# Kernel optimization log

Measured on AMD Instinct MI355X. Metric: run time of the kernel, lower is better.

Reference implementation:

```python
import jax, jax.numpy as jnp
import numpy as np

B, N, H, L = 4, 200, 128, 3
HH = H // 2
VOC_E_IN, VOC_E_OUT, NODE_DIM = 3, 2, 2
EPS_BN = 1e-5


def masked_bn(x, m, gamma, beta):
    """BatchNorm1d (batch stats, no running stats) applied only to masked positions.
    x: (..., H), m: (...) float mask. Unmasked entries pass through unchanged."""
    mm = m[..., None]
    cnt = jnp.sum(m)
    axes = tuple(range(x.ndim - 1))
    mean = jnp.sum(x * mm, axis=axes) / cnt
    var = jnp.sum(((x - mean) ** 2) * mm, axis=axes) / cnt  # biased, as BatchNorm1d
    xn = (x - mean) * jax.lax.rsqrt(var + EPS_BN) * gamma + beta
    return jnp.where(mm > 0, xn, x)


def gcn_layer(x, e, mask, sq_mask, p, i):
    # EdgeFeatures: e_ij = U*e_ij + V*x_i + V*x_j (V*x masked)
    Ue = jnp.einsum('bijh,hk->bijk', e, p['eU_w'][i]) + p['eU_b'][i]
    Vx_e = mask[..., None] * (jnp.einsum('bnh,hk->bnk', x, p['eV_w'][i]) + p['eV_b'][i])
    e_tmp = Ue + Vx_e[:, :, None, :] + Vx_e[:, None, :, :]
    gate = jax.nn.sigmoid(e_tmp)
    # NodeFeatures (mean aggregation)
    Ux = mask[..., None] * (jnp.einsum('bnh,hk->bnk', x, p['nU_w'][i]) + p['nU_b'][i])
    Vx = mask[..., None] * (jnp.einsum('bnh,hk->bnk', x, p['nV_w'][i]) + p['nV_b'][i])
    gate_m = gate * sq_mask[..., None]
    agg = jnp.einsum('bijh,bjh->bih', gate_m, Vx)
    denom = jnp.sum(gate_m, axis=2)
    x_tmp = Ux + agg / (1e-20 + denom)
    # masked batchnorm + ReLU + residual
    e_bn = masked_bn(e_tmp, sq_mask, p['bnE_g'][i], p['bnE_b'][i])
    x_bn = masked_bn(x_tmp, mask, p['bnN_g'][i], p['bnN_b'][i])
    return x + jax.nn.relu(x_bn), e + jax.nn.relu(e_bn)


def forward(x_edges, x_edges_values, x_nodes_coord, mask, p):
    x = jnp.einsum('bnd,dh->bnh', x_nodes_coord, p['w_coord'])          # (B,N,H)
    e_val = x_edges_values[..., None] * p['w_eval'][0]                  # (B,N,N,HH)
    e_tag = p['emb_edge'][x_edges]                                      # (B,N,N,HH)
    e = jnp.concatenate([e_val, e_tag], axis=-1)                        # (B,N,N,H)
    sq_mask = mask[:, :, None] * mask[:, None, :]
    for i in range(L):
        x, e = gcn_layer(x, e, mask, sq_mask, p, i)
    # MLP on edges (mlp_layers=2 -> one hidden ReLU layer)
    h = jax.nn.relu(jnp.einsum('bijh,hk->bijk', e, p['mlp_U_w']) + p['mlp_U_b'])
    y = jnp.einsum('bijh,hk->bijk', h, p['mlp_V_w']) + p['mlp_V_b']     # (B,N,N,2)
    return y


def setup_inputs() -> dict:
    key = jax.random.key(0)
    ks = jax.random.split(key, 32)
    x_edges = jax.random.randint(ks[0], (B, N, N), 0, VOC_E_IN)
    x_edges_values = jax.random.uniform(ks[1], (B, N, N), dtype=jnp.float32)
    x_nodes_coord = jax.random.uniform(ks[2], (B, N, NODE_DIM), dtype=jnp.float32)
    # prefix mask: variable graph sizes padded to N (as ConvTSP builds)
    lens = jax.random.randint(ks[3], (B,), N // 2, N + 1)
    mask = (jnp.arange(N)[None, :] < lens[:, None]).astype(jnp.float32)
    s = 1.0 / np.sqrt(H)
    inp = dict(x_edges=x_edges, x_edges_values=x_edges_values,
               x_nodes_coord=x_nodes_coord, mask=mask,
               w_coord=jax.random.normal(ks[4], (NODE_DIM, H)) * 0.5,
               w_eval=jax.random.normal(ks[5], (1, HH)) * 0.5,
               emb_edge=jax.random.normal(ks[6], (VOC_E_IN, HH)) * 0.5,
               eU_w=jax.random.normal(ks[7], (L, H, H)) * s,
               eU_b=jnp.zeros((L, H)),
               eV_w=jax.random.normal(ks[8], (L, H, H)) * s,
               eV_b=jnp.zeros((L, H)),
               nU_w=jax.random.normal(ks[9], (L, H, H)) * s,
               nU_b=jnp.zeros((L, H)),
               nV_w=jax.random.normal(ks[10], (L, H, H)) * s,
               nV_b=jnp.zeros((L, H)),
               bnE_g=jnp.ones((L, H)), bnE_b=jnp.zeros((L, H)),
               bnN_g=jnp.ones((L, H)), bnN_b=jnp.zeros((L, H)),
               mlp_U_w=jax.random.normal(ks[11], (H, H)) * s,
               mlp_U_b=jnp.zeros((H,)),
               mlp_V_w=jax.random.normal(ks[12], (H, VOC_E_OUT)) * s,
               mlp_V_b=jnp.zeros((VOC_E_OUT,)))
    return inp


def reference(x_edges, x_edges_values, x_nodes_coord, mask,
              w_coord, w_eval, emb_edge,
              eU_w, eU_b, eV_w, eV_b, nU_w, nU_b, nV_w, nV_b,
              bnE_g, bnE_b, bnN_g, bnN_b,
              mlp_U_w, mlp_U_b, mlp_V_w, mlp_V_b):
    p = dict(w_coord=w_coord, w_eval=w_eval, emb_edge=emb_edge,
             eU_w=eU_w, eU_b=eU_b, eV_w=eV_w, eV_b=eV_b,
             nU_w=nU_w, nU_b=nU_b, nV_w=nV_w, nV_b=nV_b,
             bnE_g=bnE_g, bnE_b=bnE_b, bnN_g=bnN_g, bnN_b=bnN_b,
             mlp_U_w=mlp_U_w, mlp_U_b=mlp_U_b, mlp_V_w=mlp_V_w, mlp_V_b=mlp_V_b)
    return forward(x_edges, x_edges_values, x_nodes_coord, mask, p)
```

## Files before the change

kernel.cpp:

```cpp
#include <hip/hip_runtime.h>
#include <hip/hip_bf16.h>


typedef __hip_bfloat16 bf16;
typedef __attribute__((ext_vector_type(8))) short short8_t;
typedef __attribute__((ext_vector_type(4))) float f32x4;

#define B_ 4
#define N_ 200
#define H_ 128
#define BN_ (B_ * N_)
#define MT_ 13
#define MROWS_ 208

__device__ __forceinline__ unsigned short f2b(float f) {
  unsigned int i = __float_as_uint(f);
  i = (i + 0x7fffu + ((i >> 16) & 1u)) >> 16;
  return (unsigned short)i;
}
__device__ __forceinline__ float b2f16(unsigned short u) {
  return __uint_as_float((unsigned int)u << 16);
}


__global__ __launch_bounds__(128) void k_init_x(
    const float* __restrict__ coord, const float* __restrict__ w_coord,
    float* __restrict__ x) {
  int bi = blockIdx.x, h = threadIdx.x;
  float c0 = coord[bi * 2 + 0], c1 = coord[bi * 2 + 1];
  x[(size_t)bi * H_ + h] = c0 * w_coord[h] + c1 * w_coord[H_ + h];
}

__global__ __launch_bounds__(256) void k_cnt(const float* __restrict__ mask,
                                             float* __restrict__ cnts) {
  int t = threadIdx.x, b = t >> 6, l = t & 63;
  float s = 0.f;
  for (int n = l; n < N_; n += 64) s += mask[b * N_ + n];
#pragma unroll
  for (int d = 1; d < 64; d <<= 1) s += __shfl_xor(s, d);
  __shared__ float ms[B_];
  if (l == 0) ms[b] = s;
  __syncthreads();
  if (t == 0) {
    float cn = 0.f, ce = 0.f;
    for (int k = 0; k < B_; ++k) { cn += ms[k]; ce += ms[k] * ms[k]; }
    cnts[0] = cn; cnts[1] = ce;
  }
}

__global__ __launch_bounds__(256) void k_prep_w(const float* __restrict__ eUw,
                                                const float* __restrict__ mUw,
                                                bf16* __restrict__ WT) {
  int blk = blockIdx.x;
  const float* src = (blk < 3) ? (eUw + (size_t)blk * H_ * H_) : mUw;
  bf16* dst = WT + (size_t)blk * H_ * H_;
  for (int q = threadIdx.x; q < H_ * H_; q += 256) {
    int out = q >> 7, in = q & 127;
    dst[q] = __float2bfloat16(src[in * H_ + out]);
  }
}


__global__ __launch_bounds__(128) void k_node_lin(
    const float* __restrict__ x, const float* __restrict__ eVw,
    const float* __restrict__ eVb, const float* __restrict__ nUw,
    const float* __restrict__ nUb, const float* __restrict__ nVw,
    const float* __restrict__ nVb, const float* __restrict__ mask,
    float* __restrict__ Vxe, float* __restrict__ Ux, float* __restrict__ Vx) {
  __shared__ float xr[H_];
  int bi = blockIdx.x, h = threadIdx.x;
  xr[h] = x[(size_t)bi * H_ + h];
  __syncthreads();
  float m = mask[bi];
  float a = 0.f, bvv = 0.f, c = 0.f;
#pragma unroll 4
  for (int k = 0; k < H_; ++k) {
    float xv = xr[k];
    a   = fmaf(xv, eVw[k * H_ + h], a);
    bvv = fmaf(xv, nUw[k * H_ + h], bvv);
    c   = fmaf(xv, nVw[k * H_ + h], c);
  }
  Vxe[(size_t)bi * H_ + h] = m * (a + eVb[h]);
  Ux[(size_t)bi * H_ + h]  = m * (bvv + nUb[h]);
  Vx[(size_t)bi * H_ + h]  = m * (c + nVb[h]);
}


#define LDS_PUT(SA, ROW, K0, V)                                            \
  {                                                                        \
    unsigned int p0 = ((unsigned int)f2b((V).y) << 16) | f2b((V).x);       \
    unsigned int p1 = ((unsigned int)f2b((V).w) << 16) | f2b((V).z);       \
    unsigned long long pk = ((unsigned long long)p1 << 32) | p0;           \
    int byo = ((ROW) << 8) + ((((K0) * 2)) ^ (((ROW) & 7) << 4));          \
    *(unsigned long long*)((SA) + byo) = pk;                               \
  }


template <int MODE>
__global__ __launch_bounds__(256, 3) void k_edge(
    float* __restrict__ e, bf16* __restrict__ etmp,
    const float* __restrict__ ssPrev, const int* __restrict__ xe,
    const float* __restrict__ ev, const float* __restrict__ w_eval,
    const float* __restrict__ emb, const bf16* __restrict__ WT,
    const float* __restrict__ eUb, const float* __restrict__ Vxe,
    const float* __restrict__ Vx, const float* __restrict__ Ux,
    const float* __restrict__ mask, float* __restrict__ xtmp,
    float* __restrict__ sums) {
  __shared__ __align__(16) char sA[MROWS_ * 256];
  const int bi = blockIdx.x;
  const int b = bi / N_;
  const int t = threadIdx.x;
  const int lane = t & 63;
  const int w = t >> 6;
  const float mask_i = mask[bi];

  const int n0 = w << 5;
  const int colA = n0 + (lane & 15);
  const int colB = colA + 16;
  const int kgrp = (lane >> 4) << 3;
  short8_t bfA[4], bfB[4];
  {
    const short* w0 = (const short*)WT + colA * H_ + kgrp;
    const short* w1 = (const short*)WT + colB * H_ + kgrp;
#pragma unroll
    for (int kk = 0; kk < 4; ++kk) {
      bfA[kk] = *(const short8_t*)(w0 + kk * 32);
      bfB[kk] = *(const short8_t*)(w1 + kk * 32);
    }
  }

  {
    float* eb = e + (size_t)bi * N_ * H_;
    const unsigned short* tb =
        (const unsigned short*)etmp + (size_t)bi * N_ * H_;
    for (int q4 = t; q4 < MROWS_ * 32; q4 += 256) {
      int row = q4 >> 5, k0 = (q4 & 31) << 2;
      float4 v = make_float4(0.f, 0.f, 0.f, 0.f);
      if (row < N_) {
        if (MODE == 0) {
          if (k0 < 64) {
            float evv = ev[bi * N_ + row];
            v.x = evv * w_eval[k0 + 0];
            v.y = evv * w_eval[k0 + 1];
            v.z = evv * w_eval[k0 + 2];
            v.w = evv * w_eval[k0 + 3];
          } else {
            v = *(const float4*)(emb + xe[bi * N_ + row] * 64 + (k0 - 64));
          }
        } else {
          v = *(const float4*)(eb + row * H_ + k0);
          ushort4 tv = *(const ushort4*)(tb + row * H_ + k0);
          float mj = mask[b * N_ + row];
          bool msk = (mask_i * mj) > 0.f;
          float4 sc = *(const float4*)(ssPrev + k0);
          float4 sh = *(const float4*)(ssPrev + H_ + k0);
          float f0 = b2f16(tv.x), f1 = b2f16(tv.y);
          float f2 = b2f16(tv.z), f3 = b2f16(tv.w);
          v.x += fmaxf(msk ? fmaf(f0, sc.x, sh.x) : f0, 0.f);
          v.y += fmaxf(msk ? fmaf(f1, sc.y, sh.y) : f1, 0.f);
          v.z += fmaxf(msk ? fmaf(f2, sc.z, sh.z) : f2, 0.f);
          v.w += fmaxf(msk ? fmaf(f3, sc.w, sh.w) : f3, 0.f);
        }
        *(float4*)(eb + row * H_ + k0) = v;
      }
      LDS_PUT(sA, row, k0, v)
    }
  }
  __syncthreads();

  const float add0 = eUb[colA] + Vxe[(size_t)bi * H_ + colA];
  const float add1 = eUb[colB] + Vxe[(size_t)bi * H_ + colB];
  const float* VxeB = Vxe + (size_t)b * N_ * H_;
  const float* VxB  = Vx  + (size_t)b * N_ * H_;

  float agg0 = 0.f, agg1 = 0.f, den0 = 0.f, den1 = 0.f;
  float s1a = 0.f, s1b = 0.f, s2a = 0.f, s2b = 0.f;
  const int kb = (lane >> 4) << 4;

  for (int mt = 0; mt < MT_; ++mt) {
    f32x4 acc0 = {0.f, 0.f, 0.f, 0.f}, acc1 = {0.f, 0.f, 0.f, 0.f};
    int ra = mt * 16 + (lane & 15);
#pragma unroll
    for (int kk = 0; kk < 4; ++kk) {
      int ko = kk * 64 + kb;
      short8_t av = *(const short8_t*)(sA + (ra << 8) + (ko ^ ((ra & 7) << 4)));
      acc0 = __builtin_amdgcn_mfma_f32_16x16x32_bf16(av, bfA[kk], acc0, 0, 0, 0);
      acc1 = __builtin_amdgcn_mfma_f32_16x16x32_bf16(av, bfB[kk], acc1, 0, 0, 0);
    }
#pragma unroll
    for (int r = 0; r < 4; ++r) {
      int j = mt * 16 + ((lane >> 4) << 2) + r;
      bool valid = (j < N_);
      float mj = valid ? mask[b * N_ + j] : 0.f;
      float sqm = mask_i * mj;
      float vj0 = valid ? VxeB[(size_t)j * H_ + colA] : 0.f;
      float vj1 = valid ? VxeB[(size_t)j * H_ + colB] : 0.f;
      float t0 = acc0[r] + add0 + vj0;
      float t1 = acc1[r] + add1 + vj1;
      if (valid) {
        size_t o = ((size_t)bi * N_ + j) * H_;
        etmp[o + colA] = __float2bfloat16(t0);
        etmp[o + colB] = __float2bfloat16(t1);
      }
      float g0 = sqm / (1.f + __expf(-t0));
      float g1 = sqm / (1.f + __expf(-t1));
      float vx0 = valid ? VxB[(size_t)j * H_ + colA] : 0.f;
      float vx1 = valid ? VxB[(size_t)j * H_ + colB] : 0.f;
      agg0 = fmaf(g0, vx0, agg0);
      agg1 = fmaf(g1, vx1, agg1);
      den0 += g0; den1 += g1;
      s1a = fmaf(t0, sqm, s1a);
      s1b = fmaf(t1, sqm, s1b);
      s2a = fmaf(t0 * sqm, t0, s2a);
      s2b = fmaf(t1 * sqm, t1, s2b);
    }
  }
#pragma unroll
  for (int d = 16; d <= 32; d <<= 1) {
    agg0 += __shfl_xor(agg0, d); agg1 += __shfl_xor(agg1, d);
    den0 += __shfl_xor(den0, d); den1 += __shfl_xor(den1, d);
    s1a += __shfl_xor(s1a, d);   s1b += __shfl_xor(s1b, d);
    s2a += __shfl_xor(s2a, d);   s2b += __shfl_xor(s2b, d);
  }
  if ((lane >> 4) == 0) {
    atomicAdd(&sums[colA], s1a);
    atomicAdd(&sums[colB], s1b);
    atomicAdd(&sums[H_ + colA], s2a);
    atomicAdd(&sums[H_ + colB], s2b);
    float xt0 = Ux[(size_t)bi * H_ + colA] + agg0 / (1e-20f + den0);
    float xt1 = Ux[(size_t)bi * H_ + colB] + agg1 / (1e-20f + den1);
    xtmp[(size_t)bi * H_ + colA] = xt0;
    xtmp[(size_t)bi * H_ + colB] = xt1;
    atomicAdd(&sums[2 * H_ + colA], xt0 * mask_i);
    atomicAdd(&sums[3 * H_ + colA], xt0 * xt0 * mask_i);
    atomicAdd(&sums[2 * H_ + colB], xt1 * mask_i);
    atomicAdd(&sums[3 * H_ + colB], xt1 * xt1 * mask_i);
  }
}


__global__ __launch_bounds__(128) void k_stats(
    const float* __restrict__ sums, const float* __restrict__ cnts,
    const float* __restrict__ gE, const float* __restrict__ bE,
    const float* __restrict__ gN, const float* __restrict__ bN,
    float* __restrict__ ss) {
  int h = threadIdx.x;
  float cntN = cnts[0], cntE = cnts[1];
  float mE = sums[h] / cntE;
  float vE = sums[H_ + h] / cntE - mE * mE;
  float scE = gE[h] * rsqrtf(vE + 1e-5f);
  ss[h] = scE;
  ss[H_ + h] = bE[h] - mE * scE;
  float mN = sums[2 * H_ + h] / cntN;
  float vN = sums[3 * H_ + h] / cntN - mN * mN;
  float scN = gN[h] * rsqrtf(vN + 1e-5f);
  ss[2 * H_ + h] = scN;
  ss[3 * H_ + h] = bN[h] - mN * scN;
}

__global__ __launch_bounds__(128) void k_xupd(const float* __restrict__ xtmp,
                                              const float* __restrict__ mask,
                                              const float* __restrict__ ss,
                                              float* __restrict__ x) {
  int bi = blockIdx.x, h = threadIdx.x;
  float mi = mask[bi];
  float tv = xtmp[(size_t)bi * H_ + h];
  float xn = (mi > 0.f) ? fmaf(tv, ss[2 * H_ + h], ss[3 * H_ + h]) : tv;
  x[(size_t)bi * H_ + h] += fmaxf(xn, 0.f);
}


__global__ __launch_bounds__(256, 2) void k_head(
    const float* __restrict__ e, const bf16* __restrict__ etmp,
    const float* __restrict__ ssPrev, const bf16* __restrict__ UT,
    const float* __restrict__ Ub, const float* __restrict__ Vw,
    const float* __restrict__ Vb, const float* __restrict__ mask,
    float* __restrict__ y) {
  __shared__ __align__(16) char sA[MROWS_ * 256];
  __shared__ float part[4][MROWS_][2];
  const int bi = blockIdx.x;
  const int b = bi / N_;
  const int t = threadIdx.x;
  const int lane = t & 63;
  const int w = t >> 6;
  const float mask_i = mask[bi];

  const int n0 = w << 5;
  const int colA = n0 + (lane & 15);
  const int colB = colA + 16;
  const int kgrp = (lane >> 4) << 3;
  short8_t bfA[4], bfB[4];
  {
    const short* w0 = (const short*)UT + colA * H_ + kgrp;
    const short* w1 = (const short*)UT + colB * H_ + kgrp;
#pragma unroll
    for (int kk = 0; kk < 4; ++kk) {
      bfA[kk] = *(const short8_t*)(w0 + kk * 32);
      bfB[kk] = *(const short8_t*)(w1 + kk * 32);
    }
  }

  {
    const float* eb = e + (size_t)bi * N_ * H_;
    const unsigned short* tb =
        (const unsigned short*)etmp + (size_t)bi * N_ * H_;
    for (int q4 = t; q4 < MROWS_ * 32; q4 += 256) {
      int row = q4 >> 5, k0 = (q4 & 31) << 2;
      float4 v = make_float4(0.f, 0.f, 0.f, 0.f);
      if (row < N_) {
        v = *(const float4*)(eb + row * H_ + k0);
        ushort4 tv = *(const ushort4*)(tb + row * H_ + k0);
        float mj = mask[b * N_ + row];
        bool msk = (mask_i * mj) > 0.f;
        float4 sc = *(const float4*)(ssPrev + k0);
        float4 sh = *(const float4*)(ssPrev + H_ + k0);
        float f0 = b2f16(tv.x), f1 = b2f16(tv.y);
        float f2 = b2f16(tv.z), f3 = b2f16(tv.w);
        v.x += fmaxf(msk ? fmaf(f0, sc.x, sh.x) : f0, 0.f);
        v.y += fmaxf(msk ? fmaf(f1, sc.y, sh.y) : f1, 0.f);
        v.z += fmaxf(msk ? fmaf(f2, sc.z, sh.z) : f2, 0.f);
        v.w += fmaxf(msk ? fmaf(f3, sc.w, sh.w) : f3, 0.f);
      }
      LDS_PUT(sA, row, k0, v)
    }
  }
  __syncthreads();

  float bu0 = Ub[colA], bu1 = Ub[colB];
  float v00 = Vw[colA * 2], v01 = Vw[colA * 2 + 1];
  float v10 = Vw[colB * 2], v11 = Vw[colB * 2 + 1];
  const int kb = (lane >> 4) << 4;

  for (int mt = 0; mt < MT_; ++mt) {
    f32x4 acc0 = {0.f, 0.f, 0.f, 0.f}, acc1 = {0.f, 0.f, 0.f, 0.f};
    int ra = mt * 16 + (lane & 15);
#pragma unroll
    for (int kk = 0; kk < 4; ++kk) {
      int ko = kk * 64 + kb;
      short8_t av = *(const short8_t*)(sA + (ra << 8) + (ko ^ ((ra & 7) << 4)));
      acc0 = __builtin_amdgcn_mfma_f32_16x16x32_bf16(av, bfA[kk], acc0, 0, 0, 0);
      acc1 = __builtin_amdgcn_mfma_f32_16x16x32_bf16(av, bfB[kk], acc1, 0, 0, 0);
    }
#pragma unroll
    for (int r = 0; r < 4; ++r) {
      float h0v = fmaxf(acc0[r] + bu0, 0.f);
      float h1v = fmaxf(acc1[r] + bu1, 0.f);
      float p0 = h0v * v00 + h1v * v10;
      float p1 = h0v * v01 + h1v * v11;
#pragma unroll
      for (int d = 1; d < 16; d <<= 1) {
        p0 += __shfl_xor(p0, d);
        p1 += __shfl_xor(p1, d);
      }
      int j = mt * 16 + ((lane >> 4) << 2) + r;
      if ((lane & 15) == 0) { part[w][j][0] = p0; part[w][j][1] = p1; }
    }
  }
  __syncthreads();
  float vb0 = Vb[0], vb1 = Vb[1];
  for (int q = t; q < N_ * 2; q += 256) {
    int j = q >> 1, c = q & 1;
    float s = part[0][j][c] + part[1][j][c] + part[2][j][c] + part[3][j][c] +
              (c ? vb1 : vb0);
    y[((size_t)bi * N_ + j) * 2 + c] = s;
  }
}


extern "C" void kernel_launch(void* const* d_in, const int* in_sizes, int n_in,
                              void* d_out, int out_size, void* d_ws,
                              size_t ws_size, hipStream_t stream) {
  const int*   x_edges = (const int*)d_in[0];
  const float* ev      = (const float*)d_in[1];
  const float* coord   = (const float*)d_in[2];
  const float* mask    = (const float*)d_in[3];
  const float* w_coord = (const float*)d_in[4];
  const float* w_eval  = (const float*)d_in[5];
  const float* emb     = (const float*)d_in[6];
  const float* eUw = (const float*)d_in[7];
  const float* eUb = (const float*)d_in[8];
  const float* eVw = (const float*)d_in[9];
  const float* eVb = (const float*)d_in[10];
  const float* nUw = (const float*)d_in[11];
  const float* nUb = (const float*)d_in[12];
  const float* nVw = (const float*)d_in[13];
  const float* nVb = (const float*)d_in[14];
  const float* gE  = (const float*)d_in[15];
  const float* bE  = (const float*)d_in[16];
  const float* gN  = (const float*)d_in[17];
  const float* bN  = (const float*)d_in[18];
  const float* mUw = (const float*)d_in[19];
  const float* mUb = (const float*)d_in[20];
  const float* mVw = (const float*)d_in[21];
  const float* mVb = (const float*)d_in[22];

  char* ws = (char*)d_ws;
  size_t off = 0;
  auto alloc = [&](size_t bytes) {
    void* p = ws + off;
    off += (bytes + 255) & ~(size_t)255;
    return p;
  };
  float* e    = (float*)alloc((size_t)B_ * N_ * N_ * H_ * 4);
  bf16* etmp  = (bf16*)alloc((size_t)B_ * N_ * N_ * H_ * 2);
  float* x    = (float*)alloc((size_t)BN_ * H_ * 4);
  float* Vxe  = (float*)alloc((size_t)BN_ * H_ * 4);
  float* Ux   = (float*)alloc((size_t)BN_ * H_ * 4);
  float* Vx   = (float*)alloc((size_t)BN_ * H_ * 4);
  float* xtmp = (float*)alloc((size_t)BN_ * H_ * 4);
  float* sums = (float*)alloc(4 * H_ * 4);
  float* ss   = (float*)alloc(4 * H_ * 4);
  float* cnts = (float*)alloc(256);
  bf16* WT    = (bf16*)alloc((size_t)4 * H_ * H_ * 2);

  k_prep_w<<<4, 256, 0, stream>>>(eUw, mUw, WT);
  k_init_x<<<BN_, 128, 0, stream>>>(coord, w_coord, x);
  k_cnt<<<1, 256, 0, stream>>>(mask, cnts);

  for (int l = 0; l < 3; ++l) {
    size_t wo = (size_t)l * H_ * H_;
    size_t bo = (size_t)l * H_;
    hipMemsetAsync(sums, 0, 4 * H_ * 4, stream);
    k_node_lin<<<BN_, 128, 0, stream>>>(x, eVw + wo, eVb + bo, nUw + wo,
                                        nUb + bo, nVw + wo, nVb + bo, mask,
                                        Vxe, Ux, Vx);
    if (l == 0) {
      k_edge<0><<<BN_, 256, 0, stream>>>(e, etmp, ss, x_edges, ev, w_eval,
                                         emb, WT + wo, eUb + bo, Vxe, Vx, Ux,
                                         mask, xtmp, sums);
    } else {
      k_edge<1><<<BN_, 256, 0, stream>>>(e, etmp, ss, x_edges, ev, w_eval,
                                         emb, WT + wo, eUb + bo, Vxe, Vx, Ux,
                                         mask, xtmp, sums);
    }
    k_stats<<<1, 128, 0, stream>>>(sums, cnts, gE + bo, bE + bo, gN + bo,
                                   bN + bo, ss);
    if (l < 2) k_xupd<<<BN_, 128, 0, stream>>>(xtmp, mask, ss, x);
  }
  k_head<<<BN_, 256, 0, stream>>>(e, etmp, ss, WT + (size_t)3 * H_ * H_, mUb,
                                  mVw, mVb, mask, (float*)d_out);
}
```

Measured before the change: 405.3 us.

## Store edge state in bf16, recompute layer-0 edges, fuse BN stats into consumers

The edge tensor e is now stored in bf16 instead of fp32, which halves its global read and write traffic. Layer 0 no longer writes e at all; layer 1 rebuilds the initial edge embedding on the fly (MODE 2) before adding the normalized residual. The separate k_stats and k_xupd kernels and the per-layer memsets are removed. The BN scale and shift are now recomputed from the raw sums inside k_node_lin, k_edge and k_head, and the last layer skips the unused node-update work. The edge loop also prefetches the next tile's Vxe, Vx and mask values and widens the prologue to 8-element vectors, at the cost of rounding the residual edge state to bf16.

```diff
diff --git a/kernel.cpp b/kernel.cpp
--- a/kernel.cpp
+++ b/kernel.cpp
@@ -61,24 +61,40 @@
 }
 
 
+template <int UPD>
 __global__ __launch_bounds__(128) void k_node_lin(
-    const float* __restrict__ x, const float* __restrict__ eVw,
-    const float* __restrict__ eVb, const float* __restrict__ nUw,
-    const float* __restrict__ nUb, const float* __restrict__ nVw,
-    const float* __restrict__ nVb, const float* __restrict__ mask,
-    float* __restrict__ Vxe, float* __restrict__ Ux, float* __restrict__ Vx) {
+    float* __restrict__ x, const float* __restrict__ xtmp,
+    const float* __restrict__ sumsPrev, const float* __restrict__ cnts,
+    const float* __restrict__ gNp, const float* __restrict__ bNp,
+    const float* __restrict__ eVw, const float* __restrict__ eVb,
+    const float* __restrict__ nUw, const float* __restrict__ nUb,
+    const float* __restrict__ nVw, const float* __restrict__ nVb,
+    const float* __restrict__ mask, float* __restrict__ Vxe,
+    float* __restrict__ Ux, float* __restrict__ Vx) {
   __shared__ float xr[H_];
   int bi = blockIdx.x, h = threadIdx.x;
-  xr[h] = x[(size_t)bi * H_ + h];
+  float m = mask[bi];
+  float xv = x[(size_t)bi * H_ + h];
+  if (UPD) {
+    float cntN = cnts[0];
+    float mN = sumsPrev[256 + h] / cntN;
+    float vN = sumsPrev[384 + h] / cntN - mN * mN;
+    float scN = gNp[h] * rsqrtf(vN + 1e-5f);
+    float shN = bNp[h] - mN * scN;
+    float tv = xtmp[(size_t)bi * H_ + h];
+    float xn = (m > 0.f) ? fmaf(tv, scN, shN) : tv;
+    xv += fmaxf(xn, 0.f);
+    x[(size_t)bi * H_ + h] = xv;
+  }
+  xr[h] = xv;
   __syncthreads();
-  float m = mask[bi];
   float a = 0.f, bvv = 0.f, c = 0.f;
 #pragma unroll 4
   for (int k = 0; k < H_; ++k) {
-    float xv = xr[k];
-    a   = fmaf(xv, eVw[k * H_ + h], a);
-    bvv = fmaf(xv, nUw[k * H_ + h], bvv);
-    c   = fmaf(xv, nVw[k * H_ + h], c);
+    float kx = xr[k];
+    a   = fmaf(kx, eVw[k * H_ + h], a);
+    bvv = fmaf(kx, nUw[k * H_ + h], bvv);
+    c   = fmaf(kx, nVw[k * H_ + h], c);
   }
   Vxe[(size_t)bi * H_ + h] = m * (a + eVb[h]);
   Ux[(size_t)bi * H_ + h]  = m * (bvv + nUb[h]);
@@ -86,27 +102,40 @@
 }
 
 
-#define LDS_PUT(SA, ROW, K0, V)                                            \
-  {                                                                        \
-    unsigned int p0 = ((unsigned int)f2b((V).y) << 16) | f2b((V).x);       \
-    unsigned int p1 = ((unsigned int)f2b((V).w) << 16) | f2b((V).z);       \
-    unsigned long long pk = ((unsigned long long)p1 << 32) | p0;           \
-    int byo = ((ROW) << 8) + ((((K0) * 2)) ^ (((ROW) & 7) << 4));          \
-    *(unsigned long long*)((SA) + byo) = pk;                               \
-  }
-
-
-template <int MODE>
+__device__ __forceinline__ void load_pre(int mt, int jg, int bN, float mask_i,
+                                         const float* __restrict__ mask,
+                                         const float* __restrict__ VxeB,
+                                         const float* __restrict__ VxB,
+                                         int colA, int colB, float* vj0,
+                                         float* vj1, float* vx0, float* vx1,
+                                         float* sq) {
+#pragma unroll
+  for (int r = 0; r < 4; ++r) {
+    int j = (mt << 4) + jg + r;
+    bool valid = (j < N_);
+    float mj = valid ? mask[bN + j] : 0.f;
+    sq[r] = mask_i * mj;
+    vj0[r] = valid ? VxeB[(size_t)j * H_ + colA] : 0.f;
+    vj1[r] = valid ? VxeB[(size_t)j * H_ + colB] : 0.f;
+    vx0[r] = valid ? VxB[(size_t)j * H_ + colA] : 0.f;
+    vx1[r] = valid ? VxB[(size_t)j * H_ + colB] : 0.f;
+  }
+}
+
+
+template <int MODE, bool DO_X>
 __global__ __launch_bounds__(256, 3) void k_edge(
-    float* __restrict__ e, bf16* __restrict__ etmp,
-    const float* __restrict__ ssPrev, const int* __restrict__ xe,
-    const float* __restrict__ ev, const float* __restrict__ w_eval,
-    const float* __restrict__ emb, const bf16* __restrict__ WT,
-    const float* __restrict__ eUb, const float* __restrict__ Vxe,
-    const float* __restrict__ Vx, const float* __restrict__ Ux,
-    const float* __restrict__ mask, float* __restrict__ xtmp,
-    float* __restrict__ sums) {
+    bf16* __restrict__ e, bf16* __restrict__ etmp,
+    const float* __restrict__ sumsPrev, const float* __restrict__ cnts,
+    const float* __restrict__ gEp, const float* __restrict__ bEp,
+    const int* __restrict__ xe, const float* __restrict__ ev,
+    const float* __restrict__ w_eval, const float* __restrict__ emb,
+    const bf16* __restrict__ WT, const float* __restrict__ eUb,
+    const float* __restrict__ Vxe, const float* __restrict__ Vx,
+    const float* __restrict__ Ux, const float* __restrict__ mask,
+    float* __restrict__ xtmp, float* __restrict__ sumsCur) {
   __shared__ __align__(16) char sA[MROWS_ * 256];
+  __shared__ float ssE_s[256];
   const int bi = blockIdx.x;
   const int b = bi / N_;
   const int t = threadIdx.x;
@@ -114,8 +143,17 @@
   const int w = t >> 6;
   const float mask_i = mask[bi];
 
-  const int n0 = w << 5;
-  const int colA = n0 + (lane & 15);
+  if (MODE != 0) {
+    int h = t & 127;
+    float cntE = cnts[1];
+    float mE = sumsPrev[h] / cntE;
+    float vE = sumsPrev[128 + h] / cntE - mE * mE;
+    float scE = gEp[h] * rsqrtf(vE + 1e-5f);
+    ssE_s[t] = (t < 128) ? scE : (bEp[h] - mE * scE);
+    __syncthreads();
+  }
+
+  const int colA = (w << 5) + (lane & 15);
   const int colB = colA + 16;
   const int kgrp = (lane >> 4) << 3;
   short8_t bfA[4], bfB[4];
@@ -130,40 +168,79 @@
   }
 
   {
-    float* eb = e + (size_t)bi * N_ * H_;
+    const int k0 = (t & 15) << 3;
+    const int lr0 = t >> 4;
+    float scr[8], shr[8], we[8];
+    if (MODE != 0) {
+#pragma unroll
+      for (int c = 0; c < 8; ++c) {
+        scr[c] = ssE_s[k0 + c];
+        shr[c] = ssE_s[128 + k0 + c];
+      }
+    }
+    if ((MODE == 0 || MODE == 2) && k0 < 64) {
+#pragma unroll
+      for (int c = 0; c < 8; ++c) we[c] = w_eval[k0 + c];
+    }
+    unsigned short* eb = (unsigned short*)e + (size_t)bi * N_ * H_;
     const unsigned short* tb =
         (const unsigned short*)etmp + (size_t)bi * N_ * H_;
-    for (int q4 = t; q4 < MROWS_ * 32; q4 += 256) {
-      int row = q4 >> 5, k0 = (q4 & 31) << 2;
-      float4 v = make_float4(0.f, 0.f, 0.f, 0.f);
+#pragma unroll
+    for (int n = 0; n < 13; ++n) {
+      int row = lr0 + (n << 4);
+      float v[8];
+#pragma unroll
+      for (int c = 0; c < 8; ++c) v[c] = 0.f;
       if (row < N_) {
-        if (MODE == 0) {
+        if (MODE == 0 || MODE == 2) {
           if (k0 < 64) {
             float evv = ev[bi * N_ + row];
-            v.x = evv * w_eval[k0 + 0];
-            v.y = evv * w_eval[k0 + 1];
-            v.z = evv * w_eval[k0 + 2];
-            v.w = evv * w_eval[k0 + 3];
+#pragma unroll
+            for (int c = 0; c < 8; ++c) v[c] = evv * we[c];
           } else {
-            v = *(const float4*)(emb + xe[bi * N_ + row] * 64 + (k0 - 64));
+            const float* em = emb + xe[bi * N_ + row] * 64 + (k0 - 64);
+            float4 a4 = *(const float4*)em;
+            float4 b4 = *(const float4*)(em + 4);
+            v[0] = a4.x; v[1] = a4.y; v[2] = a4.z; v[3] = a4.w;
+            v[4] = b4.x; v[5] = b4.y; v[6] = b4.z; v[7] = b4.w;
           }
         } else {
-          v = *(const float4*)(eb + row * H_ + k0);
-          ushort4 tv = *(const ushort4*)(tb + row * H_ + k0);
+          uint4 e8 = *(const uint4*)(eb + row * H_ + k0);
+          v[0] = b2f16((unsigned short)e8.x);
+          v[1] = b2f16((unsigned short)(e8.x >> 16));
+          v[2] = b2f16((unsigned short)e8.y);
+          v[3] = b2f16((unsigned short)(e8.y >> 16));
+          v[4] = b2f16((unsigned short)e8.z);
+          v[5] = b2f16((unsigned short)(e8.z >> 16));
+          v[6] = b2f16((unsigned short)e8.w);
+          v[7] = b2f16((unsigned short)(e8.w >> 16));
+        }
+        if (MODE != 0) {
+          uint4 t8 = *(const uint4*)(tb + row * H_ + k0);
           float mj = mask[b * N_ + row];
           bool msk = (mask_i * mj) > 0.f;
-          float4 sc = *(const float4*)(ssPrev + k0);
-          float4 sh = *(const float4*)(ssPrev + H_ + k0);
-          float f0 = b2f16(tv.x), f1 = b2f16(tv.y);
-          float f2 = b2f16(tv.z), f3 = b2f16(tv.w);
-          v.x += fmaxf(msk ? fmaf(f0, sc.x, sh.x) : f0, 0.f);
-          v.y += fmaxf(msk ? fmaf(f1, sc.y, sh.y) : f1, 0.f);
-          v.z += fmaxf(msk ? fmaf(f2, sc.z, sh.z) : f2, 0.f);
-          v.w += fmaxf(msk ? fmaf(f3, sc.w, sh.w) : f3, 0.f);
+          unsigned short tu[8] = {
+              (unsigned short)t8.x, (unsigned short)(t8.x >> 16),
+              (unsigned short)t8.y, (unsigned short)(t8.y >> 16),
+              (unsigned short)t8.z, (unsigned short)(t8.z >> 16),
+              (unsigned short)t8.w, (unsigned short)(t8.w >> 16)};
+#pragma unroll
+          for (int c = 0; c < 8; ++c) {
+            float f = b2f16(tu[c]);
+            float xn = msk ? fmaf(f, scr[c], shr[c]) : f;
+            v[c] += fmaxf(xn, 0.f);
+          }
         }
-        *(float4*)(eb + row * H_ + k0) = v;
       }
-      LDS_PUT(sA, row, k0, v)
+      uint4 pk;
+      pk.x = ((unsigned int)f2b(v[1]) << 16) | f2b(v[0]);
+      pk.y = ((unsigned int)f2b(v[3]) << 16) | f2b(v[2]);
+      pk.z = ((unsigned int)f2b(v[5]) << 16) | f2b(v[4]);
+      pk.w = ((unsigned int)f2b(v[7]) << 16) | f2b(v[6]);
+      if (MODE != 0 && row < N_)
+        *(uint4*)(eb + row * H_ + k0) = pk;
+      int byo = (row << 8) + ((k0 * 2) ^ ((row & 7) << 4));
+      *(uint4*)(sA + byo) = pk;
     }
   }
   __syncthreads();
@@ -172,14 +249,22 @@
   const float add1 = eUb[colB] + Vxe[(size_t)bi * H_ + colB];
   const float* VxeB = Vxe + (size_t)b * N_ * H_;
   const float* VxB  = Vx  + (size_t)b * N_ * H_;
+  const int bN = b * N_;
+  const int jg = (lane >> 4) << 2;
+  const int kb = (lane >> 4) << 4;
 
   float agg0 = 0.f, agg1 = 0.f, den0 = 0.f, den1 = 0.f;
   float s1a = 0.f, s1b = 0.f, s2a = 0.f, s2b = 0.f;
-  const int kb = (lane >> 4) << 4;
-
+
+  float cvj0[4], cvj1[4], cvx0[4], cvx1[4], csq[4];
+  float nvj0[4], nvj1[4], nvx0[4], nvx1[4], nsq[4];
+  load_pre(0, jg, bN, mask_i, mask, VxeB, VxB, colA, colB, cvj0, cvj1, cvx0,
+           cvx1, csq);
+
+#pragma unroll
   for (int mt = 0; mt < MT_; ++mt) {
     f32x4 acc0 = {0.f, 0.f, 0.f, 0.f}, acc1 = {0.f, 0.f, 0.f, 0.f};
-    int ra = mt * 16 + (lane & 15);
+    int ra = (mt << 4) + (lane & 15);
 #pragma unroll
     for (int kk = 0; kk < 4; ++kk) {
       int ko = kk * 64 + kb;
@@ -187,33 +272,36 @@
       acc0 = __builtin_amdgcn_mfma_f32_16x16x32_bf16(av, bfA[kk], acc0, 0, 0, 0);
       acc1 = __builtin_amdgcn_mfma_f32_16x16x32_bf16(av, bfB[kk], acc1, 0, 0, 0);
     }
+    if (mt < MT_ - 1)
+      load_pre(mt + 1, jg, bN, mask_i, mask, VxeB, VxB, colA, colB, nvj0,
+               nvj1, nvx0, nvx1, nsq);
 #pragma unroll
     for (int r = 0; r < 4; ++r) {
-      int j = mt * 16 + ((lane >> 4) << 2) + r;
-      bool valid = (j < N_);
-      float mj = valid ? mask[b * N_ + j] : 0.f;
-      float sqm = mask_i * mj;
-      float vj0 = valid ? VxeB[(size_t)j * H_ + colA] : 0.f;
-      float vj1 = valid ? VxeB[(size_t)j * H_ + colB] : 0.f;
-      float t0 = acc0[r] + add0 + vj0;
-      float t1 = acc1[r] + add1 + vj1;
-      if (valid) {
+      int j = (mt << 4) + jg + r;
+      float sqm = csq[r];
+      float t0 = acc0[r] + add0 + cvj0[r];
+      float t1 = acc1[r] + add1 + cvj1[r];
+      if (j < N_) {
         size_t o = ((size_t)bi * N_ + j) * H_;
-        etmp[o + colA] = __float2bfloat16(t0);
-        etmp[o + colB] = __float2bfloat16(t1);
+        ((unsigned short*)etmp)[o + colA] = f2b(t0);
+        ((unsigned short*)etmp)[o + colB] = f2b(t1);
       }
       float g0 = sqm / (1.f + __expf(-t0));
       float g1 = sqm / (1.f + __expf(-t1));
-      float vx0 = valid ? VxB[(size_t)j * H_ + colA] : 0.f;
-      float vx1 = valid ? VxB[(size_t)j * H_ + colB] : 0.f;
-      agg0 = fmaf(g0, vx0, agg0);
-      agg1 = fmaf(g1, vx1, agg1);
+      agg0 = fmaf(g0, cvx0[r], agg0);
+      agg1 = fmaf(g1, cvx1[r], agg1);
       den0 += g0; den1 += g1;
       s1a = fmaf(t0, sqm, s1a);
       s1b = fmaf(t1, sqm, s1b);
       s2a = fmaf(t0 * sqm, t0, s2a);
       s2b = fmaf(t1 * sqm, t1, s2b);
     }
+#pragma unroll
+    for (int r = 0; r < 4; ++r) {
+      cvj0[r] = nvj0[r]; cvj1[r] = nvj1[r];
+      cvx0[r] = nvx0[r]; cvx1[r] = nvx1[r];
+      csq[r] = nsq[r];
+    }
   }
 #pragma unroll
   for (int d = 16; d <= 32; d <<= 1) {
@@ -223,61 +311,34 @@
     s2a += __shfl_xor(s2a, d);   s2b += __shfl_xor(s2b, d);
   }
   if ((lane >> 4) == 0) {
-    atomicAdd(&sums[colA], s1a);
-    atomicAdd(&sums[colB], s1b);
-    atomicAdd(&sums[H_ + colA], s2a);
-    atomicAdd(&sums[H_ + colB], s2b);
-    float xt0 = Ux[(size_t)bi * H_ + colA] + agg0 / (1e-20f + den0);
-    float xt1 = Ux[(size_t)bi * H_ + colB] + agg1 / (1e-20f + den1);
-    xtmp[(size_t)bi * H_ + colA] = xt0;
-    xtmp[(size_t)bi * H_ + colB] = xt1;
-    atomicAdd(&sums[2 * H_ + colA], xt0 * mask_i);
-    atomicAdd(&sums[3 * H_ + colA], xt0 * xt0 * mask_i);
-    atomicAdd(&sums[2 * H_ + colB], xt1 * mask_i);
-    atomicAdd(&sums[3 * H_ + colB], xt1 * xt1 * mask_i);
-  }
-}
-
-
-__global__ __launch_bounds__(128) void k_stats(
-    const float* __restrict__ sums, const float* __restrict__ cnts,
-    const float* __restrict__ gE, const float* __restrict__ bE,
-    const float* __restrict__ gN, const float* __restrict__ bN,
-    float* __restrict__ ss) {
-  int h = threadIdx.x;
-  float cntN = cnts[0], cntE = cnts[1];
-  float mE = sums[h] / cntE;
-  float vE = sums[H_ + h] / cntE - mE * mE;
-  float scE = gE[h] * rsqrtf(vE + 1e-5f);
-  ss[h] = scE;
-  ss[H_ + h] = bE[h] - mE * scE;
-  float mN = sums[2 * H_ + h] / cntN;
-  float vN = sums[3 * H_ + h] / cntN - mN * mN;
-  float scN = gN[h] * rsqrtf(vN + 1e-5f);
-  ss[2 * H_ + h] = scN;
-  ss[3 * H_ + h] = bN[h] - mN * scN;
-}
-
-__global__ __launch_bounds__(128) void k_xupd(const float* __restrict__ xtmp,
-                                              const float* __restrict__ mask,
-                                              const float* __restrict__ ss,
-                                              float* __restrict__ x) {
-  int bi = blockIdx.x, h = threadIdx.x;
-  float mi = mask[bi];
-  float tv = xtmp[(size_t)bi * H_ + h];
-  float xn = (mi > 0.f) ? fmaf(tv, ss[2 * H_ + h], ss[3 * H_ + h]) : tv;
-  x[(size_t)bi * H_ + h] += fmaxf(xn, 0.f);
+    atomicAdd(&sumsCur[colA], s1a);
+    atomicAdd(&sumsCur[colB], s1b);
+    atomicAdd(&sumsCur[128 + colA], s2a);
+    atomicAdd(&sumsCur[128 + colB], s2b);
+    if (DO_X) {
+      float xt0 = Ux[(size_t)bi * H_ + colA] + agg0 / (1e-20f + den0);
+      float xt1 = Ux[(size_t)bi * H_ + colB] + agg1 / (1e-20f + den1);
+      xtmp[(size_t)bi * H_ + colA] = xt0;
+      xtmp[(size_t)bi * H_ + colB] = xt1;
+      atomicAdd(&sumsCur[256 + colA], xt0 * mask_i);
+      atomicAdd(&sumsCur[384 + colA], xt0 * xt0 * mask_i);
+      atomicAdd(&sumsCur[256 + colB], xt1 * mask_i);
+      atomicAdd(&sumsCur[384 + colB], xt1 * xt1 * mask_i);
+    }
+  }
 }
 
 
 __global__ __launch_bounds__(256, 2) void k_head(
-    const float* __restrict__ e, const bf16* __restrict__ etmp,
-    const float* __restrict__ ssPrev, const bf16* __restrict__ UT,
-    const float* __restrict__ Ub, const float* __restrict__ Vw,
-    const float* __restrict__ Vb, const float* __restrict__ mask,
-    float* __restrict__ y) {
+    const bf16* __restrict__ e, const bf16* __restrict__ etmp,
+    const float* __restrict__ sumsPrev, const float* __restrict__ cnts,
+    const float* __restrict__ gEp, const float* __restrict__ bEp,
+    const bf16* __restrict__ UT, const float* __restrict__ Ub,
+    const float* __restrict__ Vw, const float* __restrict__ Vb,
+    const float* __restrict__ mask, float* __restrict__ y) {
   __shared__ __align__(16) char sA[MROWS_ * 256];
   __shared__ float part[4][MROWS_][2];
+  __shared__ float ssE_s[256];
   const int bi = blockIdx.x;
   const int b = bi / N_;
   const int t = threadIdx.x;
@@ -285,8 +346,17 @@
   const int w = t >> 6;
   const float mask_i = mask[bi];
 
-  const int n0 = w << 5;
-  const int colA = n0 + (lane & 15);
+  {
+    int h = t & 127;
+    float cntE = cnts[1];
+    float mE = sumsPrev[h] / cntE;
+    float vE = sumsPrev[128 + h] / cntE - mE * mE;
+    float scE = gEp[h] * rsqrtf(vE + 1e-5f);
+    ssE_s[t] = (t < 128) ? scE : (bEp[h] - mE * scE);
+    __syncthreads();
+  }
+
+  const int colA = (w << 5) + (lane & 15);
   const int colB = colA + 16;
   const int kgrp = (lane >> 4) << 3;
   short8_t bfA[4], bfB[4];
@@ -301,27 +371,52 @@
   }
 
   {
-    const float* eb = e + (size_t)bi * N_ * H_;
+    const int k0 = (t & 15) << 3;
+    const int lr0 = t >> 4;
+    float scr[8], shr[8];
+#pragma unroll
+    for (int c = 0; c < 8; ++c) {
+      scr[c] = ssE_s[k0 + c];
+      shr[c] = ssE_s[128 + k0 + c];
+    }
+    const unsigned short* eb = (const unsigned short*)e + (size_t)bi * N_ * H_;
     const unsigned short* tb =
         (const unsigned short*)etmp + (size_t)bi * N_ * H_;
-    for (int q4 = t; q4 < MROWS_ * 32; q4 += 256) {
-      int row = q4 >> 5, k0 = (q4 & 31) << 2;
-      float4 v = make_float4(0.f, 0.f, 0.f, 0.f);
+#pragma unroll
+    for (int n = 0; n < 13; ++n) {
+      int row = lr0 + (n << 4);
+      float v[8];
+#pragma unroll
+      for (int c = 0; c < 8; ++c) v[c] = 0.f;
       if (row < N_) {
-        v = *(const float4*)(eb + row * H_ + k0);
-        ushort4 tv = *(const ushort4*)(tb + row * H_ + k0);
+        uint4 e8 = *(const uint4*)(eb + row * H_ + k0);
+        uint4 t8 = *(const uint4*)(tb + row * H_ + k0);
         float mj = mask[b * N_ + row];
         bool msk = (mask_i * mj) > 0.f;
-        float4 sc = *(const float4*)(ssPrev + k0);
-        float4 sh = *(const float4*)(ssPrev + H_ + k0);
-        float f0 = b2f16(tv.x), f1 = b2f16(tv.y);
-        float f2 = b2f16(tv.z), f3 = b2f16(tv.w);
-        v.x += fmaxf(msk ? fmaf(f0, sc.x, sh.x) : f0, 0.f);
-        v.y += fmaxf(msk ? fmaf(f1, sc.y, sh.y) : f1, 0.f);
-        v.z += fmaxf(msk ? fmaf(f2, sc.z, sh.z) : f2, 0.f);
-        v.w += fmaxf(msk ? fmaf(f3, sc.w, sh.w) : f3, 0.f);
+        unsigned short eu[8] = {
+            (unsigned short)e8.x, (unsigned short)(e8.x >> 16),
+            (unsigned short)e8.y, (unsigned short)(e8.y >> 16),
+            (unsigned short)e8.z, (unsigned short)(e8.z >> 16),
+            (unsigned short)e8.w, (unsigned short)(e8.w >> 16)};
+        unsigned short tu[8] = {
+            (unsigned short)t8.x, (unsigned short)(t8.x >> 16),
+            (unsigned short)t8.y, (unsigned short)(t8.y >> 16),
+            (unsigned short)t8.z, (unsigned short)(t8.z >> 16),
+            (unsigned short)t8.w, (unsigned short)(t8.w >> 16)};
+#pragma unroll
+        for (int c = 0; c < 8; ++c) {
+          float f = b2f16(tu[c]);
+          float xn = msk ? fmaf(f, scr[c], shr[c]) : f;
+          v[c] = b2f16(eu[c]) + fmaxf(xn, 0.f);
+        }
       }
-      LDS_PUT(sA, row, k0, v)
+      uint4 pk;
+      pk.x = ((unsigned int)f2b(v[1]) << 16) | f2b(v[0]);
+      pk.y = ((unsigned int)f2b(v[3]) << 16) | f2b(v[2]);
+      pk.z = ((unsigned int)f2b(v[5]) << 16) | f2b(v[4]);
+      pk.w = ((unsigned int)f2b(v[7]) << 16) | f2b(v[6]);
+      int byo = (row << 8) + ((k0 * 2) ^ ((row & 7) << 4));
+      *(uint4*)(sA + byo) = pk;
     }
   }
   __syncthreads();
@@ -333,7 +428,7 @@
 
   for (int mt = 0; mt < MT_; ++mt) {
     f32x4 acc0 = {0.f, 0.f, 0.f, 0.f}, acc1 = {0.f, 0.f, 0.f, 0.f};
-    int ra = mt * 16 + (lane & 15);
+    int ra = (mt << 4) + (lane & 15);
 #pragma unroll
     for (int kk = 0; kk < 4; ++kk) {
       int ko = kk * 64 + kb;
@@ -352,8 +447,8 @@
         p0 += __shfl_xor(p0, d);
         p1 += __shfl_xor(p1, d);
       }
-      int j = mt * 16 + ((lane >> 4) << 2) + r;
-      if ((lane & 15) == 0) { part[w][j][0] = p0; part[w][j][1] = p1; }
+      int jl = (mt << 4) + ((lane >> 4) << 2) + r;
+      if ((lane & 15) == 0) { part[w][jl][0] = p0; part[w][jl][1] = p1; }
     }
   }
   __syncthreads();
@@ -401,42 +496,46 @@
     off += (bytes + 255) & ~(size_t)255;
     return p;
   };
-  float* e    = (float*)alloc((size_t)B_ * N_ * N_ * H_ * 4);
+  bf16* e     = (bf16*)alloc((size_t)B_ * N_ * N_ * H_ * 2);
   bf16* etmp  = (bf16*)alloc((size_t)B_ * N_ * N_ * H_ * 2);
   float* x    = (float*)alloc((size_t)BN_ * H_ * 4);
   float* Vxe  = (float*)alloc((size_t)BN_ * H_ * 4);
   float* Ux   = (float*)alloc((size_t)BN_ * H_ * 4);
   float* Vx   = (float*)alloc((size_t)BN_ * H_ * 4);
   float* xtmp = (float*)alloc((size_t)BN_ * H_ * 4);
-  float* sums = (float*)alloc(4 * H_ * 4);
-  float* ss   = (float*)alloc(4 * H_ * 4);
+  float* sums = (float*)alloc(3 * 512 * 4);
   float* cnts = (float*)alloc(256);
   bf16* WT    = (bf16*)alloc((size_t)4 * H_ * H_ * 2);
 
+  hipMemsetAsync(sums, 0, 3 * 512 * 4, stream);
   k_prep_w<<<4, 256, 0, stream>>>(eUw, mUw, WT);
   k_init_x<<<BN_, 128, 0, stream>>>(coord, w_coord, x);
   k_cnt<<<1, 256, 0, stream>>>(mask, cnts);
 
-  for (int l = 0; l < 3; ++l) {
-    size_t wo = (size_t)l * H_ * H_;
-    size_t bo = (size_t)l * H_;
-    hipMemsetAsync(sums, 0, 4 * H_ * 4, stream);
-    k_node_lin<<<BN_, 128, 0, stream>>>(x, eVw + wo, eVb + bo, nUw + wo,
-                                        nUb + bo, nVw + wo, nVb + bo, mask,
-                                        Vxe, Ux, Vx);
-    if (l == 0) {
-      k_edge<0><<<BN_, 256, 0, stream>>>(e, etmp, ss, x_edges, ev, w_eval,
-                                         emb, WT + wo, eUb + bo, Vxe, Vx, Ux,
-                                         mask, xtmp, sums);
-    } else {
-      k_edge<1><<<BN_, 256, 0, stream>>>(e, etmp, ss, x_edges, ev, w_eval,
-                                         emb, WT + wo, eUb + bo, Vxe, Vx, Ux,
-                                         mask, xtmp, sums);
-    }
-    k_stats<<<1, 128, 0, stream>>>(sums, cnts, gE + bo, bE + bo, gN + bo,
-                                   bN + bo, ss);
-    if (l < 2) k_xupd<<<BN_, 128, 0, stream>>>(xtmp, mask, ss, x);
-  }
-  k_head<<<BN_, 256, 0, stream>>>(e, etmp, ss, WT + (size_t)3 * H_ * H_, mUb,
+  float* sums0 = sums;
+  float* sums1 = sums + 512;
+  float* sums2 = sums + 1024;
+
+  k_node_lin<0><<<BN_, 128, 0, stream>>>(
+      x, xtmp, sums0, cnts, gN, bN, eVw, eVb, nUw, nUb, nVw, nVb, mask, Vxe,
+      Ux, Vx);
+  k_edge<0, true><<<BN_, 256, 0, stream>>>(
+      e, etmp, sums0, cnts, gE, bE, x_edges, ev, w_eval, emb, WT, eUb, Vxe,
+      Vx, Ux, mask, xtmp, sums0);
+  k_node_lin<1><<<BN_, 128, 0, stream>>>(
+      x, xtmp, sums0, cnts, gN, bN, eVw + H_ * H_, eVb + H_, nUw + H_ * H_,
+      nUb + H_, nVw + H_ * H_, nVb + H_, mask, Vxe, Ux, Vx);
+  k_edge<2, true><<<BN_, 256, 0, stream>>>(
+      e, etmp, sums0, cnts, gE, bE, x_edges, ev, w_eval, emb, WT + H_ * H_,
+      eUb + H_, Vxe, Vx, Ux, mask, xtmp, sums1);
+  k_node_lin<1><<<BN_, 128, 0, stream>>>(
+      x, xtmp, sums1, cnts, gN + H_, bN + H_, eVw + 2 * H_ * H_,
+      eVb + 2 * H_, nUw + 2 * H_ * H_, nUb + 2 * H_, nVw + 2 * H_ * H_,
+      nVb + 2 * H_, mask, Vxe, Ux, Vx);
+  k_edge<1, false><<<BN_, 256, 0, stream>>>(
+      e, etmp, sums1, cnts, gE + H_, bE + H_, x_edges, ev, w_eval, emb,
+      WT + 2 * H_ * H_, eUb + 2 * H_, Vxe, Vx, Ux, mask, xtmp, sums2);
+  k_head<<<BN_, 256, 0, stream>>>(e, etmp, sums2, cnts, gE + 2 * H_,
+                                  bE + 2 * H_, WT + (size_t)3 * H_ * H_, mUb,
                                   mVw, mVb, mask, (float*)d_out);
 }
```

New measurement: 472.5 us. 1.17x slower.
